# Kernel tuning notes

Measured on AMD Instinct MI355X. Metric: run time of the kernel, lower is better.

Reference implementation:

```python
import jax, jax.numpy as jnp
import numpy as np

PROJ = 8192     # projDim
THRESH = 1e-8   # numerical-stability epsilon for signed sqrt
L2_EPS = 1e-12  # eps of torch F.normalize


def setup_inputs() -> dict:
    key = jax.random.key(0)
    k1, k2, k3, k4, k5 = jax.random.split(key, 5)
    B, C, H, W = 16, 512, 14, 14
    x = jax.random.normal(k1, (B, C, H, W), dtype=jnp.float32)
    h1 = jax.random.randint(k2, (C,), 0, PROJ, dtype=jnp.int32)
    h2 = jax.random.randint(k3, (C,), 0, PROJ, dtype=jnp.int32)
    s1 = (2 * jax.random.randint(k4, (C,), 0, 2) - 1).astype(jnp.float32)
    s2 = (2 * jax.random.randint(k5, (C,), 0, 2) - 1).astype(jnp.float32)
    return {"x": x, "s1": s1, "s2": s2, "h1": h1, "h2": h2}


def reference(x, s1, s2, h1, h2):
    # x: [B, C, H, W]; h*: [C] hash buckets in [0, PROJ); s*: [C] signs (+-1)
    B, C, H, W = x.shape
    x_flat = jnp.transpose(x, (0, 2, 3, 1)).reshape(-1, C)  # [N, C], N = B*H*W

    def count_sketch(s, h):
        # Equivalent to x_flat @ M with M[c, h[c]] = s[c]: scatter-add of
        # sign-weighted channels into PROJ bins.  -> [N, PROJ]
        return jax.ops.segment_sum((x_flat * s).T, h, num_segments=PROJ).T

    fft1 = jnp.fft.fft(count_sketch(s1, h1), axis=-1)
    fft2 = jnp.fft.fft(count_sketch(s2, h2), axis=-1)
    conv = jnp.fft.ifft(fft1 * fft2, axis=-1).real       # [N, PROJ]
    y = conv.reshape(B, H, W, PROJ).sum(axis=(1, 2))      # sum pool -> [B, PROJ]
    y = jnp.sign(y) * jnp.sqrt(jnp.abs(y) + THRESH)       # signed sqrt
    norm = jnp.linalg.norm(y, axis=1, keepdims=True)
    return y / jnp.maximum(norm, L2_EPS)                  # l2 normalize (dim=1)
```

## Files before the change

kernel.cpp:

```cpp
#include <hip/hip_runtime.h>
#include <math.h>

#define PROJ 8192
#define NB   16
#define NC   512
#define HW   196
#define NKC  7
#define LST  40

typedef __attribute__((ext_vector_type(8))) short bf16x8;
typedef __attribute__((ext_vector_type(4))) short short4v;
typedef __attribute__((ext_vector_type(4))) float f32x4;

__device__ __forceinline__ unsigned bf16_rne(float f) {
    unsigned u = __builtin_bit_cast(unsigned, f);
    return (u + 0x7fffu + ((u >> 16) & 1u)) >> 16;
}

__global__ __launch_bounds__(512, 2)
void cbp_gram_mfma(const float* __restrict__ x,
                   const float* __restrict__ s1,
                   const float* __restrict__ s2,
                   const int*   __restrict__ h1,
                   const int*   __restrict__ h2,
                   float* __restrict__ ws) {
    __shared__ float sk[PROJ];
    __shared__ short Ah[128 * LST];
    __shared__ short Al[128 * LST];
    __shared__ short Bh[128 * LST];
    __shared__ short Bl[128 * LST];
    __shared__ int   lh1[128], lh2[128];
    __shared__ float lsA[128], lsB[128];

    const int tid = threadIdx.x;
    const int blk = blockIdx.x;
    const int b    = 2 * (blk & 7) + (blk >> 7);
    const int tile = (blk >> 3) & 15;
    const int I = tile >> 2, J = tile & 3;
    const int c1base = I * 128;
    const int c2base = J * 128;

    const int lane = tid & 63;
    const int wave = tid >> 6;
    const int quad = lane >> 4;
    const int l15  = lane & 15;
    const int wr   = (wave >> 1) * 32;
    const int wc   = (wave & 1) * 64;

    for (int i = tid; i < PROJ; i += 512) sk[i] = 0.f;
    if (tid < 128) {
        lh1[tid] = h1[c1base + tid];  lsA[tid] = s1[c1base + tid];
        lh2[tid] = h2[c2base + tid];  lsB[tid] = s2[c2base + tid];
    }

    const float* xa = x + ((size_t)b * NC + c1base) * HW;
    const float* xb = x + ((size_t)b * NC + c2base) * HW;

    f32x4 acc[2][4];
#pragma unroll
    for (int i = 0; i < 2; ++i)
#pragma unroll
        for (int j = 0; j < 4; ++j) acc[i][j] = (f32x4){0.f, 0.f, 0.f, 0.f};

    const int sr0 = tid >> 3;
    const int sq  = tid & 7;

    float4 pa[2], pb[2];
    {
        const int kk = 4 * sq;
        const bool ok = (kk + 3 < HW);
#pragma unroll
        for (int h = 0; h < 2; ++h) {
            const int r = sr0 + 64 * h;
            pa[h] = ok ? *(const float4*)&xa[r * HW + kk] : (float4){0.f,0.f,0.f,0.f};
            pb[h] = ok ? *(const float4*)&xb[r * HW + kk] : (float4){0.f,0.f,0.f,0.f};
        }
    }

    for (int kc = 0; kc < NKC; ++kc) {
        __syncthreads();
#pragma unroll
        for (int h = 0; h < 2; ++h) {
            const int r = sr0 + 64 * h;
            const float sA = lsA[r], sB = lsB[r];
            const float fa[4] = {pa[h].x*sA, pa[h].y*sA, pa[h].z*sA, pa[h].w*sA};
            const float fb[4] = {pb[h].x*sB, pb[h].y*sB, pb[h].z*sB, pb[h].w*sB};
            short4v ah, al, bh, bl;
#pragma unroll
            for (int c = 0; c < 4; ++c) {
                const unsigned ha_ = bf16_rne(fa[c]);
                ah[c] = (short)ha_;
                al[c] = (short)bf16_rne(fa[c] - __builtin_bit_cast(float, ha_ << 16));
                const unsigned hb_ = bf16_rne(fb[c]);
                bh[c] = (short)hb_;
                bl[c] = (short)bf16_rne(fb[c] - __builtin_bit_cast(float, hb_ << 16));
            }
            *(short4v*)&Ah[r * LST + 4 * sq] = ah;
            *(short4v*)&Al[r * LST + 4 * sq] = al;
            *(short4v*)&Bh[r * LST + 4 * sq] = bh;
            *(short4v*)&Bl[r * LST + 4 * sq] = bl;
        }
        if (kc + 1 < NKC) {
            const int kk = (kc + 1) * 32 + 4 * sq;
            const bool ok = (kk + 3 < HW);
#pragma unroll
            for (int h = 0; h < 2; ++h) {
                const int r = sr0 + 64 * h;
                pa[h] = ok ? *(const float4*)&xa[r * HW + kk] : (float4){0.f,0.f,0.f,0.f};
                pb[h] = ok ? *(const float4*)&xb[r * HW + kk] : (float4){0.f,0.f,0.f,0.f};
            }
        }
        __syncthreads();

        bf16x8 ahf[2], alf[2], bhf[4], blf[4];
#pragma unroll
        for (int i = 0; i < 2; ++i) {
            const int ra = wr + i * 16 + l15;
            ahf[i] = *(const bf16x8*)&Ah[ra * LST + quad * 8];
            alf[i] = *(const bf16x8*)&Al[ra * LST + quad * 8];
        }
#pragma unroll
        for (int j = 0; j < 4; ++j) {
            const int rb = wc + j * 16 + l15;
            bhf[j] = *(const bf16x8*)&Bh[rb * LST + quad * 8];
            blf[j] = *(const bf16x8*)&Bl[rb * LST + quad * 8];
        }
#pragma unroll
        for (int i = 0; i < 2; ++i)
#pragma unroll
            for (int j = 0; j < 4; ++j) {
                acc[i][j] = __builtin_amdgcn_mfma_f32_16x16x32_bf16(ahf[i], bhf[j], acc[i][j], 0, 0, 0);
                acc[i][j] = __builtin_amdgcn_mfma_f32_16x16x32_bf16(ahf[i], blf[j], acc[i][j], 0, 0, 0);
                acc[i][j] = __builtin_amdgcn_mfma_f32_16x16x32_bf16(alf[i], bhf[j], acc[i][j], 0, 0, 0);
            }
    }
    __syncthreads();

#pragma unroll
    for (int i = 0; i < 2; ++i) {
        const int lr0 = wr + i * 16 + quad * 4;
#pragma unroll
        for (int j = 0; j < 4; ++j) {
            const int h2v = lh2[wc + j * 16 + l15];
#pragma unroll
            for (int rg = 0; rg < 4; ++rg) {
                const int bin = (lh1[lr0 + rg] + h2v) & (PROJ - 1);
                atomicAdd(&sk[bin], acc[i][j][rg]);
            }
        }
    }
    __syncthreads();

    float4* dst = (float4*)(ws + (size_t)blk * PROJ);
    const float4* src = (const float4*)sk;
    for (int i = tid; i < PROJ / 4; i += 512) dst[i] = src[i];
}

__global__ __launch_bounds__(256)
void cbp_reduce(const float* __restrict__ ws, float* __restrict__ y,
                float* __restrict__ ssqp) {
    const int blk = blockIdx.x;
    const int b   = blk >> 5;
    const int seg = blk & 31;
    const int tid = threadIdx.x;
    const int bin = seg * 256 + tid;

    const int pbase = ((b & 1) << 7) | (b >> 1);
    float s = 0.f;
#pragma unroll
    for (int t = 0; t < 16; ++t)
        s += ws[(size_t)(pbase | (t << 3)) * PROJ + bin];

    const float m = sqrtf(fabsf(s) + 1e-8f);
    const float o = (s > 0.f) ? m : (s < 0.f ? -m : 0.f);
    y[b * PROJ + bin] = o;

    __shared__ float red[256];
    red[tid] = o * o;
    __syncthreads();
#pragma unroll
    for (int st = 128; st >= 1; st >>= 1) {
        if (tid < st) red[tid] += red[tid + st];
        __syncthreads();
    }
    if (tid == 0) ssqp[blk] = red[0];
}

__global__ __launch_bounds__(256)
void cbp_normalize(float* __restrict__ y, const float* __restrict__ ssqp) {
    const int b   = blockIdx.x >> 1;
    const int off = (blockIdx.x & 1) * 4096;
    const int tid = threadIdx.x;
    float ssq = 0.f;
#pragma unroll
    for (int i = 0; i < 32; ++i) ssq += ssqp[b * 32 + i];
    const float inv = 1.0f / fmaxf(sqrtf(ssq), 1e-12f);

    float4* row = (float4*)&y[(size_t)b * PROJ + off];
#pragma unroll
    for (int j = 0; j < 4; ++j) {
        float4 v = row[j * 256 + tid];
        v.x *= inv; v.y *= inv; v.z *= inv; v.w *= inv;
        row[j * 256 + tid] = v;
    }
}

extern "C" void kernel_launch(void* const* d_in, const int* in_sizes, int n_in,
                              void* d_out, int out_size, void* d_ws, size_t ws_size,
                              hipStream_t stream) {
    const float* x  = (const float*)d_in[0];
    const float* s1 = (const float*)d_in[1];
    const float* s2 = (const float*)d_in[2];
    const int*   h1 = (const int*)d_in[3];
    const int*   h2 = (const int*)d_in[4];
    float* y    = (float*)d_out;
    float* ws   = (float*)d_ws;
    float* ssqp = ws + (size_t)256 * PROJ;

    hipLaunchKernelGGL(cbp_gram_mfma, dim3(256), dim3(512), 0, stream,
                       x, s1, s2, h1, h2, ws);
    hipLaunchKernelGGL(cbp_reduce, dim3(512), dim3(256), 0, stream, ws, y, ssqp);
    hipLaunchKernelGGL(cbp_normalize, dim3(32), dim3(256), 0, stream, y, ssqp);
}
```

Measured before the change: 103.8 us.

## Load MFMA fragments directly from global memory and fuse reduce with normalize

```diff
diff --git a/kernel.cpp b/kernel.cpp
--- a/kernel.cpp
+++ b/kernel.cpp
@@ -6,10 +6,8 @@
 #define NC   512
 #define HW   196
 #define NKC  7
-#define LST  40
 
 typedef __attribute__((ext_vector_type(8))) short bf16x8;
-typedef __attribute__((ext_vector_type(4))) short short4v;
 typedef __attribute__((ext_vector_type(4))) float f32x4;
 
 __device__ __forceinline__ unsigned bf16_rne(float f) {
@@ -17,28 +15,37 @@
     return (u + 0x7fffu + ((u >> 16) & 1u)) >> 16;
 }
 
+__device__ __forceinline__ void cvt_frag(const float4 f0, const float4 f1,
+                                         const float s, bf16x8& hi, bf16x8& lo) {
+    const float f[8] = {f0.x * s, f0.y * s, f0.z * s, f0.w * s,
+                        f1.x * s, f1.y * s, f1.z * s, f1.w * s};
+    bf16x8 h, l;
+#pragma unroll
+    for (int c = 0; c < 8; ++c) {
+        const unsigned hu = bf16_rne(f[c]);
+        h[c] = (short)hu;
+        l[c] = (short)bf16_rne(f[c] - __builtin_bit_cast(float, hu << 16));
+    }
+    hi = h;
+    lo = l;
+}
+
 __global__ __launch_bounds__(512, 2)
-void cbp_gram_mfma(const float* __restrict__ x,
-                   const float* __restrict__ s1,
-                   const float* __restrict__ s2,
-                   const int*   __restrict__ h1,
-                   const int*   __restrict__ h2,
-                   float* __restrict__ ws) {
+void cbp_gram(const float* __restrict__ x,
+              const float* __restrict__ s1,
+              const float* __restrict__ s2,
+              const int*   __restrict__ h1,
+              const int*   __restrict__ h2,
+              float* __restrict__ ws) {
     __shared__ float sk[PROJ];
-    __shared__ short Ah[128 * LST];
-    __shared__ short Al[128 * LST];
-    __shared__ short Bh[128 * LST];
-    __shared__ short Bl[128 * LST];
     __shared__ int   lh1[128], lh2[128];
-    __shared__ float lsA[128], lsB[128];
 
     const int tid = threadIdx.x;
     const int blk = blockIdx.x;
     const int b    = 2 * (blk & 7) + (blk >> 7);
     const int tile = (blk >> 3) & 15;
-    const int I = tile >> 2, J = tile & 3;
-    const int c1base = I * 128;
-    const int c2base = J * 128;
+    const int c1base = (tile >> 2) * 128;
+    const int c2base = (tile & 3) * 128;
 
     const int lane = tid & 63;
     const int wave = tid >> 6;
@@ -48,92 +55,71 @@
     const int wc   = (wave & 1) * 64;
 
     for (int i = tid; i < PROJ; i += 512) sk[i] = 0.f;
-    if (tid < 128) {
-        lh1[tid] = h1[c1base + tid];  lsA[tid] = s1[c1base + tid];
-        lh2[tid] = h2[c2base + tid];  lsB[tid] = s2[c2base + tid];
-    }
+    if (tid < 128) { lh1[tid] = h1[c1base + tid]; lh2[tid] = h2[c2base + tid]; }
 
     const float* xa = x + ((size_t)b * NC + c1base) * HW;
     const float* xb = x + ((size_t)b * NC + c2base) * HW;
 
+    const float* pA[2]; float sa[2];
+#pragma unroll
+    for (int i = 0; i < 2; ++i) {
+        const int r = wr + i * 16 + l15;
+        pA[i] = xa + r * HW;
+        sa[i] = s1[c1base + r];
+    }
+    const float* pB[4]; float sb[4];
+#pragma unroll
+    for (int j = 0; j < 4; ++j) {
+        const int r = wc + j * 16 + l15;
+        pB[j] = xb + r * HW;
+        sb[j] = s2[c2base + r];
+    }
+
     f32x4 acc[2][4];
 #pragma unroll
     for (int i = 0; i < 2; ++i)
 #pragma unroll
         for (int j = 0; j < 4; ++j) acc[i][j] = (f32x4){0.f, 0.f, 0.f, 0.f};
 
-    const int sr0 = tid >> 3;
-    const int sq  = tid & 7;
-
-    float4 pa[2], pb[2];
-    {
-        const int kk = 4 * sq;
-        const bool ok = (kk + 3 < HW);
-#pragma unroll
-        for (int h = 0; h < 2; ++h) {
-            const int r = sr0 + 64 * h;
-            pa[h] = ok ? *(const float4*)&xa[r * HW + kk] : (float4){0.f,0.f,0.f,0.f};
-            pb[h] = ok ? *(const float4*)&xb[r * HW + kk] : (float4){0.f,0.f,0.f,0.f};
-        }
-    }
-
+    const float4 z4 = {0.f, 0.f, 0.f, 0.f};
+    float4 buf[2][12];
+
+#define LOADC(par, kc) do {                                                   \
+    const int kk_ = (kc) * 32 + quad * 8;                                     \
+    const bool ok0_ = (kk_ + 3) < HW, ok1_ = (kk_ + 7) < HW;                  \
+    _Pragma("unroll") for (int i_ = 0; i_ < 2; ++i_) {                        \
+        buf[par][2*i_]   = ok0_ ? *(const float4*)(pA[i_] + kk_)     : z4;    \
+        buf[par][2*i_+1] = ok1_ ? *(const float4*)(pA[i_] + kk_ + 4) : z4; }  \
+    _Pragma("unroll") for (int j_ = 0; j_ < 4; ++j_) {                        \
+        buf[par][4+2*j_]   = ok0_ ? *(const float4*)(pB[j_] + kk_)     : z4;  \
+        buf[par][4+2*j_+1] = ok1_ ? *(const float4*)(pB[j_] + kk_ + 4) : z4; }\
+} while (0)
+
+    LOADC(0, 0);
+#pragma unroll
     for (int kc = 0; kc < NKC; ++kc) {
-        __syncthreads();
-#pragma unroll
-        for (int h = 0; h < 2; ++h) {
-            const int r = sr0 + 64 * h;
-            const float sA = lsA[r], sB = lsB[r];
-            const float fa[4] = {pa[h].x*sA, pa[h].y*sA, pa[h].z*sA, pa[h].w*sA};
-            const float fb[4] = {pb[h].x*sB, pb[h].y*sB, pb[h].z*sB, pb[h].w*sB};
-            short4v ah, al, bh, bl;
-#pragma unroll
-            for (int c = 0; c < 4; ++c) {
-                const unsigned ha_ = bf16_rne(fa[c]);
-                ah[c] = (short)ha_;
-                al[c] = (short)bf16_rne(fa[c] - __builtin_bit_cast(float, ha_ << 16));
-                const unsigned hb_ = bf16_rne(fb[c]);
-                bh[c] = (short)hb_;
-                bl[c] = (short)bf16_rne(fb[c] - __builtin_bit_cast(float, hb_ << 16));
+        const int cur = kc & 1;
+        if (kc + 1 < NKC) LOADC(cur ^ 1, kc + 1);
+
+        bf16x8 ah[2], al[2], bh[4], bl[4];
+#pragma unroll
+        for (int i = 0; i < 2; ++i)
+            cvt_frag(buf[cur][2*i], buf[cur][2*i+1], sa[i], ah[i], al[i]);
+#pragma unroll
+        for (int j = 0; j < 4; ++j)
+            cvt_frag(buf[cur][4+2*j], buf[cur][4+2*j+1], sb[j], bh[j], bl[j]);
+
+#pragma unroll
+        for (int i = 0; i < 2; ++i)
+#pragma unroll
+            for (int j = 0; j < 4; ++j) {
+                acc[i][j] = __builtin_amdgcn_mfma_f32_16x16x32_bf16(ah[i], bh[j], acc[i][j], 0, 0, 0);
+                acc[i][j] = __builtin_amdgcn_mfma_f32_16x16x32_bf16(ah[i], bl[j], acc[i][j], 0, 0, 0);
+                acc[i][j] = __builtin_amdgcn_mfma_f32_16x16x32_bf16(al[i], bh[j], acc[i][j], 0, 0, 0);
             }
-            *(short4v*)&Ah[r * LST + 4 * sq] = ah;
-            *(short4v*)&Al[r * LST + 4 * sq] = al;
-            *(short4v*)&Bh[r * LST + 4 * sq] = bh;
-            *(short4v*)&Bl[r * LST + 4 * sq] = bl;
-        }
-        if (kc + 1 < NKC) {
-            const int kk = (kc + 1) * 32 + 4 * sq;
-            const bool ok = (kk + 3 < HW);
-#pragma unroll
-            for (int h = 0; h < 2; ++h) {
-                const int r = sr0 + 64 * h;
-                pa[h] = ok ? *(const float4*)&xa[r * HW + kk] : (float4){0.f,0.f,0.f,0.f};
-                pb[h] = ok ? *(const float4*)&xb[r * HW + kk] : (float4){0.f,0.f,0.f,0.f};
-            }
-        }
-        __syncthreads();
-
-        bf16x8 ahf[2], alf[2], bhf[4], blf[4];
-#pragma unroll
-        for (int i = 0; i < 2; ++i) {
-            const int ra = wr + i * 16 + l15;
-            ahf[i] = *(const bf16x8*)&Ah[ra * LST + quad * 8];
-            alf[i] = *(const bf16x8*)&Al[ra * LST + quad * 8];
-        }
-#pragma unroll
-        for (int j = 0; j < 4; ++j) {
-            const int rb = wc + j * 16 + l15;
-            bhf[j] = *(const bf16x8*)&Bh[rb * LST + quad * 8];
-            blf[j] = *(const bf16x8*)&Bl[rb * LST + quad * 8];
-        }
-#pragma unroll
-        for (int i = 0; i < 2; ++i)
-#pragma unroll
-            for (int j = 0; j < 4; ++j) {
-                acc[i][j] = __builtin_amdgcn_mfma_f32_16x16x32_bf16(ahf[i], bhf[j], acc[i][j], 0, 0, 0);
-                acc[i][j] = __builtin_amdgcn_mfma_f32_16x16x32_bf16(ahf[i], blf[j], acc[i][j], 0, 0, 0);
-                acc[i][j] = __builtin_amdgcn_mfma_f32_16x16x32_bf16(alf[i], bhf[j], acc[i][j], 0, 0, 0);
-            }
-    }
+    }
+#undef LOADC
+
     __syncthreads();
 
 #pragma unroll
@@ -156,52 +142,52 @@
     for (int i = tid; i < PROJ / 4; i += 512) dst[i] = src[i];
 }
 
-__global__ __launch_bounds__(256)
-void cbp_reduce(const float* __restrict__ ws, float* __restrict__ y,
-                float* __restrict__ ssqp) {
-    const int blk = blockIdx.x;
-    const int b   = blk >> 5;
-    const int seg = blk & 31;
+__device__ __forceinline__ float ssqrt(float s) {
+    const float m = sqrtf(fabsf(s) + 1e-8f);
+    return (s > 0.f) ? m : (s < 0.f ? -m : 0.f);
+}
+
+__global__ __launch_bounds__(512)
+void cbp_finalize(const float* __restrict__ ws, float* __restrict__ y) {
+    __shared__ float red[8];
+    const int b   = blockIdx.x;
     const int tid = threadIdx.x;
-    const int bin = seg * 256 + tid;
-
     const int pbase = ((b & 1) << 7) | (b >> 1);
-    float s = 0.f;
-#pragma unroll
-    for (int t = 0; t < 16; ++t)
-        s += ws[(size_t)(pbase | (t << 3)) * PROJ + bin];
-
-    const float m = sqrtf(fabsf(s) + 1e-8f);
-    const float o = (s > 0.f) ? m : (s < 0.f ? -m : 0.f);
-    y[b * PROJ + bin] = o;
-
-    __shared__ float red[256];
-    red[tid] = o * o;
+
+    float4 ov[4];
+    float ssq = 0.f;
+#pragma unroll
+    for (int g = 0; g < 4; ++g) {
+        const int f4 = tid + 512 * g;
+        float4 s = {0.f, 0.f, 0.f, 0.f};
+#pragma unroll
+        for (int t = 0; t < 16; ++t) {
+            const float4 v =
+                ((const float4*)(ws + (size_t)(pbase | (t << 3)) * PROJ))[f4];
+            s.x += v.x; s.y += v.y; s.z += v.z; s.w += v.w;
+        }
+        float4 o;
+        o.x = ssqrt(s.x); o.y = ssqrt(s.y); o.z = ssqrt(s.z); o.w = ssqrt(s.w);
+        ov[g] = o;
+        ssq += o.x * o.x + o.y * o.y + o.z * o.z + o.w * o.w;
+    }
+
+    float v = ssq;
+#pragma unroll
+    for (int off = 32; off >= 1; off >>= 1) v += __shfl_xor(v, off, 64);
+    if ((tid & 63) == 0) red[tid >> 6] = v;
     __syncthreads();
-#pragma unroll
-    for (int st = 128; st >= 1; st >>= 1) {
-        if (tid < st) red[tid] += red[tid + st];
-        __syncthreads();
-    }
-    if (tid == 0) ssqp[blk] = red[0];
-}
-
-__global__ __launch_bounds__(256)
-void cbp_normalize(float* __restrict__ y, const float* __restrict__ ssqp) {
-    const int b   = blockIdx.x >> 1;
-    const int off = (blockIdx.x & 1) * 4096;
-    const int tid = threadIdx.x;
-    float ssq = 0.f;
-#pragma unroll
-    for (int i = 0; i < 32; ++i) ssq += ssqp[b * 32 + i];
-    const float inv = 1.0f / fmaxf(sqrtf(ssq), 1e-12f);
-
-    float4* row = (float4*)&y[(size_t)b * PROJ + off];
-#pragma unroll
-    for (int j = 0; j < 4; ++j) {
-        float4 v = row[j * 256 + tid];
-        v.x *= inv; v.y *= inv; v.z *= inv; v.w *= inv;
-        row[j * 256 + tid] = v;
+    float tot = 0.f;
+#pragma unroll
+    for (int w = 0; w < 8; ++w) tot += red[w];
+    const float inv = 1.0f / fmaxf(sqrtf(tot), 1e-12f);
+
+    float4* yp = (float4*)(y + (size_t)b * PROJ);
+#pragma unroll
+    for (int g = 0; g < 4; ++g) {
+        float4 o = ov[g];
+        o.x *= inv; o.y *= inv; o.z *= inv; o.w *= inv;
+        yp[tid + 512 * g] = o;
     }
 }
 
@@ -213,12 +199,10 @@
     const float* s2 = (const float*)d_in[2];
     const int*   h1 = (const int*)d_in[3];
     const int*   h2 = (const int*)d_in[4];
-    float* y    = (float*)d_out;
-    float* ws   = (float*)d_ws;
-    float* ssqp = ws + (size_t)256 * PROJ;
-
-    hipLaunchKernelGGL(cbp_gram_mfma, dim3(256), dim3(512), 0, stream,
+    float* y  = (float*)d_out;
+    float* ws = (float*)d_ws;
+
+    hipLaunchKernelGGL(cbp_gram, dim3(256), dim3(512), 0, stream,
                        x, s1, s2, h1, h2, ws);
-    hipLaunchKernelGGL(cbp_reduce, dim3(512), dim3(256), 0, stream, ws, y, ssqp);
-    hipLaunchKernelGGL(cbp_normalize, dim3(32), dim3(256), 0, stream, y, ssqp);
-}
+    hipLaunchKernelGGL(cbp_finalize, dim3(16), dim3(512), 0, stream, ws, y);
+}
```

After: 106.7 us. 2.8% more time.
